# Performance work log

Hardware: AMD Instinct MI355X
Metric: run time of the kernel (lower is better)

## Reference

```python
import jax, jax.numpy as jnp
import numpy as np
from jax.ops import segment_sum
import math

N = 100_000
E = 1_600_000
D = 128          # node_feature_dim
HID = 128        # hidden_dim
H = 4            # num_heads
HD = HID // H    # head_dim


def setup_inputs() -> dict:
    key = jax.random.key(0)
    ks = jax.random.split(key, 12)
    s = 0.02
    return {
        "node_features": jax.random.normal(ks[0], (N, D), dtype=jnp.float32),
        "edge_index": jax.random.randint(ks[1], (2, E), 0, N, dtype=jnp.int32),
        "edge_weights": jax.random.uniform(ks[2], (E,), dtype=jnp.float32),
        "Wq": jax.random.normal(ks[3], (D, HID), dtype=jnp.float32) * s,
        "bq": jnp.zeros((HID,), dtype=jnp.float32),
        "Wk": jax.random.normal(ks[4], (D, HID), dtype=jnp.float32) * s,
        "bk": jnp.zeros((HID,), dtype=jnp.float32),
        "Wv": jax.random.normal(ks[5], (D, HID), dtype=jnp.float32) * s,
        "bv": jnp.zeros((HID,), dtype=jnp.float32),
        "Wo": jax.random.normal(ks[6], (HID, HID), dtype=jnp.float32) * s,
        "bo": jnp.zeros((HID,), dtype=jnp.float32),
        "We": jax.random.normal(ks[7], (H,), dtype=jnp.float32) * s,  # edge_proj weight, Linear(1, H)
        "be": jnp.zeros((H,), dtype=jnp.float32),
    }


def reference(node_features, edge_index, edge_weights,
              Wq, bq, Wk, bk, Wv, bv, Wo, bo, We, be):
    scale = math.sqrt(HD)
    Q = (node_features @ Wq + bq).reshape(N, H, HD)
    K = (node_features @ Wk + bk).reshape(N, H, HD)
    V = (node_features @ Wv + bv).reshape(N, H, HD)

    src, tgt = edge_index[0], edge_index[1]

    # per-edge attention scores (E, H)
    scores = jnp.einsum("ehd,ehd->eh", Q[tgt], K[src]) / scale
    # edge_proj: Linear(1, H) applied to edge_weights[:, None]
    scores = scores + edge_weights[:, None] * We[None, :] + be[None, :]

    # scatter softmax over target nodes
    max_scores = jnp.full((N, H), -1e9, dtype=scores.dtype).at[tgt].max(scores)
    exp_scores = jnp.exp(scores - max_scores[tgt])
    sum_exp = segment_sum(exp_scores, tgt, num_segments=N)
    probs = exp_scores / (sum_exp[tgt] + 1e-8)

    # weighted scatter-sum aggregation
    out = jnp.zeros((N, H, HD), dtype=scores.dtype).at[tgt].add(probs[:, :, None] * V[src])
    return out.reshape(N, HID) @ Wo + bo
```

## Files before the change

kernel.cpp:

```cpp
#include <hip/hip_runtime.h>

#define N_NODES 100000
#define E_EDGES 1600000

typedef unsigned short u16;
typedef unsigned int   u32;
typedef unsigned char  u8;
typedef float f32x4  __attribute__((ext_vector_type(4)));
typedef short bf16x8 __attribute__((ext_vector_type(8)));

#define NBUK 98
#define BCAP 20480
#define MBLOCKS 1563
#define ECHUNKS 391

__device__ __forceinline__ u16 f2b(float f) {
  u32 b = __float_as_uint(f);
  return (u16)((b + 0x7FFFu + ((b >> 16) & 1u)) >> 16);
}
__device__ __forceinline__ float blo(u32 u) { return __uint_as_float(u << 16); }
__device__ __forceinline__ float bhi(u32 u) { return __uint_as_float(u & 0xFFFF0000u); }

__device__ __forceinline__ u8 f2e4m3(float f) {
  u32 b = __float_as_uint(f);
  u32 s = (b >> 24) & 0x80u;
  float y = __uint_as_float(b & 0x7fffffffu) * 0x1p-120f;
  u32 u = __float_as_uint(y);
  u += 0x7FFFFu + ((u >> 20) & 1u);
  return (u8)(s | ((u >> 20) & 0x7fu));
}

__device__ __forceinline__ float e4m3_1(u32 x) {
  u32 y = ((x & 0x80u) << 24) | ((x & 0x7fu) << 20);
  return __uint_as_float(y) * 0x1p120f;
}

__device__ __forceinline__ void dec4(u32 kq, float& k0, float& k1, float& k2, float& k3) {
#if __has_builtin(__builtin_amdgcn_cvt_pk_f32_fp8)
  auto lo = __builtin_amdgcn_cvt_pk_f32_fp8((int)kq, false);
  auto hi = __builtin_amdgcn_cvt_pk_f32_fp8((int)kq, true);
  k0 = lo[0]; k1 = lo[1]; k2 = hi[0]; k3 = hi[1];
#else
  k0 = e4m3_1(kq); k1 = e4m3_1(kq >> 8); k2 = e4m3_1(kq >> 16); k3 = e4m3_1(kq >> 24);
#endif
}

template<int CTRL>
__device__ __forceinline__ float dpp_add(float d) {
  int x = __builtin_amdgcn_update_dpp(0, __float_as_int(d), CTRL, 0xf, 0xf, true);
  return d + __int_as_float(x);
}
__device__ __forceinline__ float reduce8(float d) {
  d = dpp_add<0xB1>(d);
  d = dpp_add<0x4E>(d);
  d = dpp_add<0x141>(d);
  return d;
}

__global__ __launch_bounds__(256) void setup(
    const float* __restrict__ Wq, const float* __restrict__ Wk,
    const float* __restrict__ Wv, const float* __restrict__ Wo,
    u16* __restrict__ Wt, u32* __restrict__ bcur)
{
  int tid = blockIdx.x * 256 + threadIdx.x;
  if (tid < NBUK) bcur[tid] = (u32)tid * BCAP;
  int idx = tid - NBUK;
  if (idx >= 0 && idx < 65536) {
    int mat = idx >> 14;
    int rem = idx & 16383;
    int n = rem >> 7, k = rem & 127;
    const float* W = (mat == 0) ? Wq : (mat == 1) ? Wk : (mat == 2) ? Wv : Wo;
    Wt[idx] = f2b(W[k * 128 + n]);
  }
}

__global__ __launch_bounds__(256) void qkv_pass1(
    const float* __restrict__ A, const u16* __restrict__ Wt,
    const float* __restrict__ bq, const float* __restrict__ bk,
    const float* __restrict__ bv,
    u16* __restrict__ Qb, u8* __restrict__ Kf8, u16* __restrict__ Vb16, int M,
    const int* __restrict__ ei, const float* __restrict__ ew,
    u32* __restrict__ bcur, uint2* __restrict__ stag)
{
  __shared__ __align__(16) char smem[52224];
  const int t = threadIdx.x;

  if ((int)blockIdx.x < MBLOCKS) {
    typedef u16 row136[136];
    row136* Alds = (row136*)smem;
    row136* Blds = (row136*)(smem + 17408);
    const int row0 = blockIdx.x * 64;

#pragma unroll
    for (int i = 0; i < 8; ++i) {
      int f = t + i * 256;
      int r = f >> 5, c4 = f & 31;
      int gr = row0 + r; if (gr >= M) gr = M - 1;
      float4 v = ((const float4*)(A + (size_t)gr * 128))[c4];
      u32* dst = (u32*)&Alds[r][c4 * 4];
      dst[0] = (u32)f2b(v.x) | ((u32)f2b(v.y) << 16);
      dst[1] = (u32)f2b(v.z) | ((u32)f2b(v.w) << 16);
    }

    const int lane = t & 63;
    const int mrow = lane & 15;
    const int q    = lane >> 4;
    const int m0   = (t >> 6) * 16;

    for (int m = 0; m < 3; ++m) {
      __syncthreads();
#pragma unroll
      for (int i = 0; i < 8; ++i) {
        int f = t + i * 256;
        int r = f >> 4, c8 = f & 15;
        uint4 v = ((const uint4*)(Wt + (size_t)m * 16384 + (size_t)r * 128))[c8];
        *(uint4*)&Blds[r][c8 * 8] = v;
      }
      __syncthreads();

      f32x4 acc[8];
#pragma unroll
      for (int c = 0; c < 8; ++c) acc[c] = (f32x4){0.f, 0.f, 0.f, 0.f};
#pragma unroll
      for (int kk = 0; kk < 4; ++kk) {
        const int kb = kk * 32 + q * 8;
        bf16x8 a = *(const bf16x8*)&Alds[m0 + mrow][kb];
#pragma unroll
        for (int c = 0; c < 8; ++c) {
          bf16x8 b = *(const bf16x8*)&Blds[c * 16 + mrow][kb];
          acc[c] = __builtin_amdgcn_mfma_f32_16x16x32_bf16(a, b, acc[c], 0, 0, 0);
        }
      }

      const float* bias = (m == 0) ? bq : (m == 1) ? bk : bv;
      __syncthreads();
      if (m == 1) {
        u8* Kst = (u8*)Blds;
#pragma unroll
        for (int c = 0; c < 8; ++c) {
          int gcol = c * 16 + mrow;
          float bvv = bias[gcol];
#pragma unroll
          for (int r = 0; r < 4; ++r)
            Kst[(m0 + q * 4 + r) * 144 + gcol] = f2e4m3(acc[c][r] + bvv);
        }
        __syncthreads();
#pragma unroll
        for (int i = 0; i < 2; ++i) {
          int f = t + i * 256;
          int r = f >> 3, c16 = f & 7;
          int grow = row0 + r;
          if (grow < M)
            *(uint4*)(Kf8 + (size_t)grow * 128 + c16 * 16) =
                *(const uint4*)(Kst + r * 144 + c16 * 16);
        }
      } else {
        u16* St = (u16*)Blds;
#pragma unroll
        for (int c = 0; c < 8; ++c) {
          int gcol = c * 16 + mrow;
          float bvv = bias[gcol];
#pragma unroll
          for (int r = 0; r < 4; ++r)
            St[(m0 + q * 4 + r) * 136 + gcol] = f2b(acc[c][r] + bvv);
        }
        __syncthreads();
        u16* dstM = (m == 0) ? Qb : Vb16;
#pragma unroll
        for (int i = 0; i < 4; ++i) {
          int f = t + i * 256;
          int r = f >> 4, c8 = f & 15;
          int grow = row0 + r;
          if (grow < M)
            *(uint4*)(dstM + (size_t)grow * 128 + c8 * 8) =
                *(const uint4*)(St + r * 136 + c8 * 8);
        }
      }
    }
  } else {
    u32* s_px    = (u32*)smem;
    u32* s_py    = (u32*)(smem + 16384);
    u32* s_gp    = (u32*)(smem + 32768);
    u32* s_hist  = (u32*)(smem + 49152);
    u32* s_excl  = (u32*)(smem + 49544);
    u32* s_gbase = (u32*)(smem + 49936);
    u32* s_wsum  = (u32*)(smem + 50328);

    const int base = ((int)blockIdx.x - MBLOCKS) * 4096;
    const int nv = min(4096, E_EDGES - base);

    if (t < NBUK) s_hist[t] = 0;
    __syncthreads();

    u32 tg[16], py[16];
    const int4*   src4 = (const int4*)(ei + base);
    const int4*   tgt4 = (const int4*)(ei + E_EDGES + base);
    const float4* ewv4 = (const float4*)(ew + base);
#pragma unroll
    for (int j = 0; j < 4; ++j) {
      int q4 = t + j * 256;
      bool valid = (q4 * 4) < nv;
      int qq = valid ? q4 : 0;
      int4   sv = src4[qq];
      int4   tv = tgt4[qq];
      float4 wv = ewv4[qq];
      u32* TG = &tg[j * 4];
      u32* PY = &py[j * 4];
      TG[0] = (u32)tv.x; TG[1] = (u32)tv.y; TG[2] = (u32)tv.z; TG[3] = (u32)tv.w;
      PY[0] = ((u32)sv.x << 15) | (u32)(wv.x * 32768.0f);
      PY[1] = ((u32)sv.y << 15) | (u32)(wv.y * 32768.0f);
      PY[2] = ((u32)sv.z << 15) | (u32)(wv.z * 32768.0f);
      PY[3] = ((u32)sv.w << 15) | (u32)(wv.w * 32768.0f);
      if (valid) {
        atomicAdd(&s_hist[TG[0] >> 10], 1u);
        atomicAdd(&s_hist[TG[1] >> 10], 1u);
        atomicAdd(&s_hist[TG[2] >> 10], 1u);
        atomicAdd(&s_hist[TG[3] >> 10], 1u);
      } else {
        TG[0] = TG[1] = TG[2] = TG[3] = 0xFFFFFFFFu;
      }
    }
    __syncthreads();

    {
      int v = (t < NBUK) ? (int)s_hist[t] : 0;
      int x = v;
#pragma unroll
      for (int d = 1; d < 64; d <<= 1) {
        int y = __shfl_up(x, d, 64);
        if ((t & 63) >= d) x += y;
      }
      if ((t & 63) == 63 && t < 128) s_wsum[t >> 6] = (u32)x;
      __syncthreads();
      if (t < NBUK) {
        int incl = x + ((t >= 64) ? (int)s_wsum[0] : 0);
        s_excl[t] = (u32)(incl - v);
        s_gbase[t] = (v > 0) ? atomicAdd(&bcur[t], (u32)v) : 0u;
      }
    }
    __syncthreads();
    if (t < NBUK) s_hist[t] = s_excl[t];
    __syncthreads();

#pragma unroll
    for (int i = 0; i < 16; ++i) {
      if (tg[i] != 0xFFFFFFFFu) {
        u32 bk = tg[i] >> 10;
        u32 lp = atomicAdd(&s_hist[bk], 1u);
        s_px[lp] = tg[i];
        s_py[lp] = py[i];
        s_gp[lp] = s_gbase[bk] + (lp - s_excl[bk]);
      }
    }
    __syncthreads();
    for (int s = t; s < nv; s += 256)
      stag[s_gp[s]] = make_uint2(s_px[s], s_py[s]);
  }
}

__global__ __launch_bounds__(256) void gemm_out(
    const u16* __restrict__ A, const u16* __restrict__ Wt,
    const float* __restrict__ bias, float* __restrict__ Cout, int M)
{
  __shared__ __align__(16) u16 Alds[64][136];
  __shared__ __align__(16) u16 Blds[128][136];
  const int t = threadIdx.x;
  const int row0 = blockIdx.x * 64;

#pragma unroll
  for (int i = 0; i < 4; ++i) {
    int f = t + i * 256;
    int r = f >> 4, c8 = f & 15;
    int gr = row0 + r; if (gr >= M) gr = M - 1;
    uint4 v = ((const uint4*)(A + (size_t)gr * 128))[c8];
    *(uint4*)&Alds[r][c8 * 8] = v;
  }
#pragma unroll
  for (int i = 0; i < 8; ++i) {
    int f = t + i * 256;
    int r = f >> 4, c8 = f & 15;
    uint4 v = ((const uint4*)(Wt + (size_t)r * 128))[c8];
    *(uint4*)&Blds[r][c8 * 8] = v;
  }
  __syncthreads();

  const int lane = t & 63;
  const int mrow = lane & 15;
  const int q    = lane >> 4;
  const int m0   = (t >> 6) * 16;

  f32x4 acc[8];
#pragma unroll
  for (int c = 0; c < 8; ++c) acc[c] = (f32x4){0.f, 0.f, 0.f, 0.f};
#pragma unroll
  for (int kk = 0; kk < 4; ++kk) {
    const int kb = kk * 32 + q * 8;
    bf16x8 a = *(const bf16x8*)&Alds[m0 + mrow][kb];
#pragma unroll
    for (int c = 0; c < 8; ++c) {
      bf16x8 b = *(const bf16x8*)&Blds[c * 16 + mrow][kb];
      acc[c] = __builtin_amdgcn_mfma_f32_16x16x32_bf16(a, b, acc[c], 0, 0, 0);
    }
  }

  __syncthreads();
  float* Fst = (float*)&Blds[0][0];
#pragma unroll
  for (int c = 0; c < 8; ++c) {
    int gcol = c * 16 + mrow;
    float bv = bias[gcol];
#pragma unroll
    for (int r = 0; r < 4; ++r)
      Fst[(m0 + q * 4 + r) * 132 + gcol] = acc[c][r] + bv;
  }
  __syncthreads();
#pragma unroll
  for (int i = 0; i < 8; ++i) {
    int f = t + i * 256;
    int r = f >> 5, c4 = f & 31;
    int grow = row0 + r;
    if (grow < M) {
      f32x4 vv = *(const f32x4*)(Fst + r * 132 + c4 * 4);
      __builtin_nontemporal_store(vv, (f32x4*)(Cout + (size_t)grow * 128 + c4 * 4));
    }
  }
}

__global__ __launch_bounds__(1024) void pass2_scatter(
    const u32* __restrict__ bcur, const uint2* __restrict__ stag,
    int2* __restrict__ nodeinfo, u32* __restrict__ csr)
{
  __shared__ int s_hist[1024];
  __shared__ int s_wsum[16];
  const int t = threadIdx.x;
  const int b = blockIdx.x;
  const int sb = b * BCAP;
  const int cnt = (int)bcur[b] - sb;
  const int node_base = b << 10;

  s_hist[t] = 0;
  __syncthreads();

  typedef unsigned long long u64;
  const u64* sg = (const u64*)stag;
  u32 tgr[20], pyr[20];
#pragma unroll
  for (int k = 0; k < 20; ++k) {
    int i = t + k * 1024;
    if (i < cnt) {
      u64 e = __builtin_nontemporal_load(sg + sb + i);
      tgr[k] = (u32)e & 1023u;
      pyr[k] = (u32)(e >> 32);
      atomicAdd(&s_hist[tgr[k]], 1);
    } else {
      tgr[k] = 0xFFFFFFFFu;
      pyr[k] = 0u;
    }
  }
  __syncthreads();

  int v = s_hist[t];
  int x = v;
#pragma unroll
  for (int d = 1; d < 64; d <<= 1) {
    int y = __shfl_up(x, d, 64);
    if ((t & 63) >= d) x += y;
  }
  if ((t & 63) == 63) s_wsum[t >> 6] = x;
  __syncthreads();
  if (t < 64) {
    int w = (t < 16) ? s_wsum[t] : 0;
#pragma unroll
    for (int d = 1; d < 16; d <<= 1) {
      int y = __shfl_up(w, d, 64);
      if (t >= d) w += y;
    }
    if (t < 16) s_wsum[t] = w;
  }
  __syncthreads();
  int wbase = (t >= 64) ? s_wsum[(t >> 6) - 1] : 0;
  int excl = x + wbase - v;
  int node = node_base + t;
  if (node < N_NODES) nodeinfo[node] = make_int2(sb + excl, v);
  __syncthreads();
  s_hist[t] = sb + excl;
  __syncthreads();

#pragma unroll
  for (int k = 0; k < 20; ++k) {
    if (tgr[k] != 0xFFFFFFFFu) {
      int pos = atomicAdd(&s_hist[tgr[k]], 1);
      csr[pos] = pyr[k];
    }
  }
}

__global__ __launch_bounds__(256) void gather_fused(
    const int2* __restrict__ nodeinfo, const u32* __restrict__ csr,
    u32* __restrict__ Qb32, const u8* __restrict__ Kf8,
    const u32* __restrict__ Vb,
    const float* __restrict__ We, const float* __restrict__ be)
{
  int node = blockIdx.x * 4 + (threadIdx.x >> 6);
  int l    = threadIdx.x & 63;
  int half = l >> 5;
  int hl   = l & 31;
  int h    = hl >> 3;

  const float scale = 0.17677669529663687f;
  const float eiq   = 1.0f / 32768.0f;
  uint2 qp = *(const uint2*)(Qb32 + (size_t)node * 64 + hl * 2);
  float qa = blo(qp.x) * scale, qb = bhi(qp.x) * scale;
  float qc = blo(qp.y) * scale, qd = bhi(qp.y) * scale;
  float weq = We[h] * eiq, bE = be[h];
  const u32 laneK = (u32)hl * 4;
  const u32 laneV = (u32)hl * 8;

  int2 ni = nodeinfo[node];
  int s0 = ni.x, L = ni.y;
  int npair = L >> 1;
  const u32* cp = csr + s0 + half;
  const char* Kc = (const char*)Kf8;
  const char* Vc = (const char*)Vb;

  float a0 = 0.f, a1 = 0.f, a2 = 0.f, a3 = 0.f, sum = 0.f;

  auto LDK = [&](u32 c) -> u32 {
    return *(const u32*)(Kc + (((c >> 15) << 7) + laneK));
  };
  auto LDV = [&](u32 c) -> uint2 {
    return *(const uint2*)(Vc + (((c >> 15) << 8) + laneV));
  };
  auto COMP = [&](u32 c, u32 kq, uint2 vv) {
    float k0, k1, k2, k3;
    dec4(kq, k0, k1, k2, k3);
    float d = qa * k0 + qb * k1 + qc * k2 + qd * k3;
    d = reduce8(d);
    float p = __expf(d + (float)(c & 32767u) * weq + bE);
    sum += p;
    a0 += p * blo(vv.x);
    a1 += p * bhi(vv.x);
    a2 += p * blo(vv.y);
    a3 += p * bhi(vv.y);
  };

  int i = 0;
  for (; i + 4 <= npair; i += 4) {
    u32 c0 = cp[2 * i];
    u32 c1 = cp[2 * i + 2];
    u32 c2 = cp[2 * i + 4];
    u32 c3 = cp[2 * i + 6];
    u32 k0 = LDK(c0), k1 = LDK(c1), k2 = LDK(c2), k3 = LDK(c3);
    uint2 v0 = LDV(c0), v1 = LDV(c1), v2 = LDV(c2), v3 = LDV(c3);
    COMP(c0, k0, v0);
    COMP(c1, k1, v1);
    COMP(c2, k2, v2);
    COMP(c3, k3, v3);
  }
  for (; i < npair; ++i) {
    u32 c = cp[2 * i];
    u32 kq = LDK(c);
    uint2 vv = LDV(c);
    COMP(c, kq, vv);
  }
  if (L & 1) {
    u32 c = csr[s0 + L - 1];
    u32 kq = LDK(c);
    uint2 vv = LDV(c);
    float k0, k1, k2, k3;
    dec4(kq, k0, k1, k2, k3);
    float d = qa * k0 + qb * k1 + qc * k2 + qd * k3;
    d = reduce8(d);
    float p = __expf(d + (float)(c & 32767u) * weq + bE);
    p = half ? 0.f : p;
    sum += p;
    a0 += p * blo(vv.x);
    a1 += p * bhi(vv.x);
    a2 += p * blo(vv.y);
    a3 += p * bhi(vv.y);
  }

  sum += __shfl_xor(sum, 32, 64);
  a0  += __shfl_xor(a0, 32, 64);
  a1  += __shfl_xor(a1, 32, 64);
  a2  += __shfl_xor(a2, 32, 64);
  a3  += __shfl_xor(a3, 32, 64);

  float inv = 1.f / (sum + 1e-8f);
  if (half == 0) {
    uint2 w;
    w.x = (u32)f2b(a0 * inv) | ((u32)f2b(a1 * inv) << 16);
    w.y = (u32)f2b(a2 * inv) | ((u32)f2b(a3 * inv) << 16);
    *(uint2*)(Qb32 + (size_t)node * 64 + hl * 2) = w;
  }
}

extern "C" void kernel_launch(void* const* d_in, const int* in_sizes, int n_in,
                              void* d_out, int out_size, void* d_ws, size_t ws_size,
                              hipStream_t stream) {
  const float* nf = (const float*)d_in[0];
  const int*   ei = (const int*)  d_in[1];
  const float* ew = (const float*)d_in[2];
  const float* Wq = (const float*)d_in[3];
  const float* bq = (const float*)d_in[4];
  const float* Wk = (const float*)d_in[5];
  const float* bk = (const float*)d_in[6];
  const float* Wv = (const float*)d_in[7];
  const float* bv = (const float*)d_in[8];
  const float* Wo = (const float*)d_in[9];
  const float* bo = (const float*)d_in[10];
  const float* We = (const float*)d_in[11];
  const float* be = (const float*)d_in[12];
  float* out = (float*)d_out;

  char* ws = (char*)d_ws;
  u16*  Wt  = (u16*)ws;
  u16*  Qb  = (u16*)(ws + 131072);
  u8*   Kf8 = (u8*)(Qb + (size_t)N_NODES * 128);
  u16*  Vb16 = (u16*)(Kf8 + (size_t)N_NODES * 128);
  char* p   = (char*)(Vb16 + (size_t)N_NODES * 128);
  uint2* stag = (uint2*)p;              p += (size_t)NBUK * BCAP * 8;
  u32*  csr = (u32*)p;                  p += (size_t)NBUK * BCAP * 4;
  int2* nodeinfo = (int2*)p;            p += (size_t)N_NODES * 8;
  u32*  bcur = (u32*)p;                 p += 512;

  setup<<<(NBUK + 65536 + 255) / 256, 256, 0, stream>>>(Wq, Wk, Wv, Wo, Wt, bcur);

  qkv_pass1<<<MBLOCKS + ECHUNKS, 256, 0, stream>>>(
      nf, Wt, bq, bk, bv, Qb, Kf8, Vb16, N_NODES, ei, ew, bcur, stag);

  pass2_scatter<<<NBUK, 1024, 0, stream>>>(bcur, stag, nodeinfo, csr);

  gather_fused<<<N_NODES / 4, 256, 0, stream>>>(nodeinfo, csr,
      (u32*)Qb, Kf8, (const u32*)Vb16, We, be);

  gemm_out<<<MBLOCKS, 256, 0, stream>>>(Qb, Wt + 49152, bo, out, N_NODES);
}
```

Before: 278.3 us.

## Load GEMM A-fragments directly into registers and scatter edges without LDS staging

In the QKV projection and output GEMM kernels, each lane now loads its MFMA A-operand rows straight from global memory into registers instead of staging the A tile through shared memory. This cuts shared memory per block from about 52KB to 34KB, which could allow more resident blocks. The edge bucketing branch now writes each edge straight to its global staging slot after the local atomic, dropping the LDS reorder buffers and one barrier. The cost is less coalesced global loads for A and scattered, uncoalesced staging writes.

```diff
diff --git a/kernel.cpp b/kernel.cpp
--- a/kernel.cpp
+++ b/kernel.cpp
@@ -82,30 +82,33 @@
     const int* __restrict__ ei, const float* __restrict__ ew,
     u32* __restrict__ bcur, uint2* __restrict__ stag)
 {
-  __shared__ __align__(16) char smem[52224];
+  __shared__ __align__(16) char smem[34816];
   const int t = threadIdx.x;
 
   if ((int)blockIdx.x < MBLOCKS) {
     typedef u16 row136[136];
-    row136* Alds = (row136*)smem;
-    row136* Blds = (row136*)(smem + 17408);
+    row136* Blds = (row136*)smem;
     const int row0 = blockIdx.x * 64;
-
-#pragma unroll
-    for (int i = 0; i < 8; ++i) {
-      int f = t + i * 256;
-      int r = f >> 5, c4 = f & 31;
-      int gr = row0 + r; if (gr >= M) gr = M - 1;
-      float4 v = ((const float4*)(A + (size_t)gr * 128))[c4];
-      u32* dst = (u32*)&Alds[r][c4 * 4];
-      dst[0] = (u32)f2b(v.x) | ((u32)f2b(v.y) << 16);
-      dst[1] = (u32)f2b(v.z) | ((u32)f2b(v.w) << 16);
-    }
 
     const int lane = t & 63;
     const int mrow = lane & 15;
     const int q    = lane >> 4;
     const int m0   = (t >> 6) * 16;
+
+    int gr = row0 + m0 + mrow; if (gr >= M) gr = M - 1;
+    const float4* Arow = (const float4*)(A + (size_t)gr * 128);
+    bf16x8 areg[4];
+#pragma unroll
+    for (int kk = 0; kk < 4; ++kk) {
+      float4 v0 = Arow[kk * 8 + q * 2];
+      float4 v1 = Arow[kk * 8 + q * 2 + 1];
+      union { bf16x8 v; u32 u[4]; } cv;
+      cv.u[0] = (u32)f2b(v0.x) | ((u32)f2b(v0.y) << 16);
+      cv.u[1] = (u32)f2b(v0.z) | ((u32)f2b(v0.w) << 16);
+      cv.u[2] = (u32)f2b(v1.x) | ((u32)f2b(v1.y) << 16);
+      cv.u[3] = (u32)f2b(v1.z) | ((u32)f2b(v1.w) << 16);
+      areg[kk] = cv.v;
+    }
 
     for (int m = 0; m < 3; ++m) {
       __syncthreads();
@@ -124,7 +127,7 @@
 #pragma unroll
       for (int kk = 0; kk < 4; ++kk) {
         const int kb = kk * 32 + q * 8;
-        bf16x8 a = *(const bf16x8*)&Alds[m0 + mrow][kb];
+        bf16x8 a = areg[kk];
 #pragma unroll
         for (int c = 0; c < 8; ++c) {
           bf16x8 b = *(const bf16x8*)&Blds[c * 16 + mrow][kb];
@@ -135,7 +138,7 @@
       const float* bias = (m == 0) ? bq : (m == 1) ? bk : bv;
       __syncthreads();
       if (m == 1) {
-        u8* Kst = (u8*)Blds;
+        u8* Kst = (u8*)smem;
 #pragma unroll
         for (int c = 0; c < 8; ++c) {
           int gcol = c * 16 + mrow;
@@ -155,7 +158,7 @@
                 *(const uint4*)(Kst + r * 144 + c16 * 16);
         }
       } else {
-        u16* St = (u16*)Blds;
+        u16* St = (u16*)smem;
 #pragma unroll
         for (int c = 0; c < 8; ++c) {
           int gcol = c * 16 + mrow;
@@ -178,13 +181,10 @@
       }
     }
   } else {
-    u32* s_px    = (u32*)smem;
-    u32* s_py    = (u32*)(smem + 16384);
-    u32* s_gp    = (u32*)(smem + 32768);
-    u32* s_hist  = (u32*)(smem + 49152);
-    u32* s_excl  = (u32*)(smem + 49544);
-    u32* s_gbase = (u32*)(smem + 49936);
-    u32* s_wsum  = (u32*)(smem + 50328);
+    u32* s_hist  = (u32*)smem;
+    u32* s_excl  = (u32*)(smem + 512);
+    u32* s_gbase = (u32*)(smem + 1024);
+    u32* s_wsum  = (u32*)(smem + 1536);
 
     const int base = ((int)blockIdx.x - MBLOCKS) * 4096;
     const int nv = min(4096, E_EDGES - base);
@@ -247,34 +247,23 @@
       if (tg[i] != 0xFFFFFFFFu) {
         u32 bk = tg[i] >> 10;
         u32 lp = atomicAdd(&s_hist[bk], 1u);
-        s_px[lp] = tg[i];
-        s_py[lp] = py[i];
-        s_gp[lp] = s_gbase[bk] + (lp - s_excl[bk]);
-      }
-    }
-    __syncthreads();
-    for (int s = t; s < nv; s += 256)
-      stag[s_gp[s]] = make_uint2(s_px[s], s_py[s]);
+        u32 dest = s_gbase[bk] + (lp - s_excl[bk]);
+        stag[dest] = make_uint2(tg[i], py[i]);
+      }
+    }
   }
 }
 
 __global__ __launch_bounds__(256) void gemm_out(
-    const u16* __restrict__ A, const u16* __restrict__ Wt,
+    const u16* __restrict__ Aq, const u16* __restrict__ Wt,
     const float* __restrict__ bias, float* __restrict__ Cout, int M)
 {
-  __shared__ __align__(16) u16 Alds[64][136];
-  __shared__ __align__(16) u16 Blds[128][136];
+  __shared__ __align__(16) char smem[34816];
+  typedef u16 row136[136];
+  row136* Blds = (row136*)smem;
   const int t = threadIdx.x;
   const int row0 = blockIdx.x * 64;
 
-#pragma unroll
-  for (int i = 0; i < 4; ++i) {
-    int f = t + i * 256;
-    int r = f >> 4, c8 = f & 15;
-    int gr = row0 + r; if (gr >= M) gr = M - 1;
-    uint4 v = ((const uint4*)(A + (size_t)gr * 128))[c8];
-    *(uint4*)&Alds[r][c8 * 8] = v;
-  }
 #pragma unroll
   for (int i = 0; i < 8; ++i) {
     int f = t + i * 256;
@@ -282,20 +271,27 @@
     uint4 v = ((const uint4*)(Wt + (size_t)r * 128))[c8];
     *(uint4*)&Blds[r][c8 * 8] = v;
   }
-  __syncthreads();
 
   const int lane = t & 63;
   const int mrow = lane & 15;
   const int q    = lane >> 4;
   const int m0   = (t >> 6) * 16;
 
+  int gr = row0 + m0 + mrow; if (gr >= M) gr = M - 1;
+  const bf16x8* Arow = (const bf16x8*)(Aq + (size_t)gr * 128);
+  bf16x8 areg[4];
+#pragma unroll
+  for (int kk = 0; kk < 4; ++kk) areg[kk] = Arow[kk * 4 + q];
+
+  __syncthreads();
+
   f32x4 acc[8];
 #pragma unroll
   for (int c = 0; c < 8; ++c) acc[c] = (f32x4){0.f, 0.f, 0.f, 0.f};
 #pragma unroll
   for (int kk = 0; kk < 4; ++kk) {
     const int kb = kk * 32 + q * 8;
-    bf16x8 a = *(const bf16x8*)&Alds[m0 + mrow][kb];
+    bf16x8 a = areg[kk];
 #pragma unroll
     for (int c = 0; c < 8; ++c) {
       bf16x8 b = *(const bf16x8*)&Blds[c * 16 + mrow][kb];
@@ -304,7 +300,7 @@
   }
 
   __syncthreads();
-  float* Fst = (float*)&Blds[0][0];
+  float* Fst = (float*)smem;
 #pragma unroll
   for (int c = 0; c < 8; ++c) {
     int gcol = c * 16 + mrow;
```

Measured after the change: 276.1 us. About the same (-0.8%).
